# Optimization experiments

Measured on AMD Instinct MI355X. Metric: run time of the kernel, lower is better.

## Reference

```python
import jax, jax.numpy as jnp
import numpy as np


def gcn_conv(x, W, b, src, dst, n):
    # GCNConv with self-loops and symmetric normalization:
    # out_i = sum_{j in N(i)} (deg_i*deg_j)^{-1/2} (x_j W) + deg_i^{-1} (x_i W) + b
    h = x @ W                                   # [n, H]
    deg = jnp.zeros((n,), h.dtype).at[dst].add(1.0) + 1.0  # +1 self-loop
    dinv = jax.lax.rsqrt(deg)                   # deg^{-1/2}
    norm = dinv[src] * dinv[dst]                # [E]
    msg = h[src] * norm[:, None]                # [E, H] gathered/scaled messages
    agg = jax.ops.segment_sum(msg, dst, num_segments=n)
    agg = agg + h * (dinv * dinv)[:, None]      # self-loop contribution
    return agg + b


def global_mean_pool(x, batch, num_graphs):
    s = jax.ops.segment_sum(x, batch, num_segments=num_graphs)
    cnt = jax.ops.segment_sum(jnp.ones((x.shape[0],), x.dtype), batch, num_segments=num_graphs)
    return s / jnp.maximum(cnt, 1.0)[:, None]


def setup_inputs() -> dict:
    key = jax.random.key(0)
    ks = jax.random.split(key, 8)
    N, E, F, H, G = 100000, 1600000, 128, 128, 512
    x = jax.random.normal(ks[0], (N, F), dtype=jnp.float32)
    edge_index = jax.random.randint(ks[1], (2, E), 0, N, dtype=jnp.int64)
    batch = jnp.sort(jax.random.randint(ks[2], (N,), 0, G, dtype=jnp.int64))
    W1 = jax.random.normal(ks[3], (F, H), dtype=jnp.float32) / np.sqrt(F)
    b1 = jnp.zeros((H,), jnp.float32)
    W2 = jax.random.normal(ks[4], (H, H), dtype=jnp.float32) / np.sqrt(H)
    b2 = jnp.zeros((H,), jnp.float32)
    Wlin = jax.random.normal(ks[5], (H, 1), dtype=jnp.float32) / np.sqrt(H)
    blin = jnp.zeros((1,), jnp.float32)
    return {"x": x, "W1": W1, "b1": b1, "W2": W2, "b2": b2,
            "Wlin": Wlin, "blin": blin,
            "edge_index": edge_index, "batch": batch, "num_graphs": G}


def reference(x, W1, b1, W2, b2, Wlin, blin, edge_index, batch, num_graphs):
    n = x.shape[0]
    src, dst = edge_index[0], edge_index[1]
    h = jax.nn.relu(gcn_conv(x, W1, b1, src, dst, n))
    h = jax.nn.relu(gcn_conv(h, W2, b2, src, dst, n))
    g = global_mean_pool(h, batch, num_graphs)   # [G, H]
    return g @ Wlin + blin                       # [G, 1]
```

## Files before the change

kernel.cpp:

```cpp
#include <hip/hip_runtime.h>
#include <hip/hip_bf16.h>


#define NBS 7
#define NPB 128
#define PART_TILE 4096
#define BCAP 3072

typedef __attribute__((ext_vector_type(8))) short short8;
typedef __attribute__((ext_vector_type(4))) float f32x4;

__device__ __forceinline__ float bf2f(unsigned short u) {
    return __uint_as_float(((unsigned int)u) << 16);
}
__device__ __forceinline__ unsigned short f2bf(float f) {
    unsigned int u = __float_as_uint(f);
    return (unsigned short)((u + 0x7FFFu + ((u >> 16) & 1u)) >> 16);
}
__device__ __forceinline__ short8 pack_bf8(f32x4 a, f32x4 b) {
    short8 s;
    s[0] = (short)f2bf(a.x); s[1] = (short)f2bf(a.y);
    s[2] = (short)f2bf(a.z); s[3] = (short)f2bf(a.w);
    s[4] = (short)f2bf(b.x); s[5] = (short)f2bf(b.y);
    s[6] = (short)f2bf(b.z); s[7] = (short)f2bf(b.w);
    return s;
}
__device__ __forceinline__ void acc8(int4 v, float* a) {
    a[0] += __uint_as_float(((unsigned int)v.x) << 16);
    a[1] += __uint_as_float(((unsigned int)v.x) & 0xFFFF0000u);
    a[2] += __uint_as_float(((unsigned int)v.y) << 16);
    a[3] += __uint_as_float(((unsigned int)v.y) & 0xFFFF0000u);
    a[4] += __uint_as_float(((unsigned int)v.z) << 16);
    a[5] += __uint_as_float(((unsigned int)v.z) & 0xFFFF0000u);
    a[6] += __uint_as_float(((unsigned int)v.w) << 16);
    a[7] += __uint_as_float(((unsigned int)v.w) & 0xFFFF0000u);
}
__device__ __forceinline__ unsigned int pack2(float x, float y) {
    return (unsigned int)f2bf(x) | ((unsigned int)f2bf(y) << 16);
}


__global__ __launch_bounds__(256) void partition_kernel(const int* __restrict__ src,
                                                        const int* __restrict__ dst, int E,
                                                        int* __restrict__ bcur,
                                                        unsigned int* __restrict__ pairs,
                                                        int B) {
    __shared__ int h[1024];
    __shared__ int rankbase[1024];
    int t = threadIdx.x;
    int tile0 = blockIdx.x * PART_TILE;
    for (int i = t; i < B; i += 256) h[i] = 0;
    __syncthreads();

    int bk[16];
    int rk[16];
    unsigned int pk[16];
#pragma unroll
    for (int j = 0; j < 16; ++j) {
        int idx = tile0 + j * 256 + t;
        bk[j] = -1;
        if (idx < E) {
            int d = dst[idx];
            int s = src[idx];
            bk[j] = d >> NBS;
            pk[j] = ((unsigned int)(d & (NPB - 1)) << 23) | (unsigned int)s;
            rk[j] = atomicAdd(&h[bk[j]], 1);
        }
    }
    __syncthreads();
    for (int i = t; i < B; i += 256) rankbase[i] = h[i] ? atomicAdd(&bcur[i], h[i]) : 0;
    __syncthreads();
#pragma unroll
    for (int j = 0; j < 16; ++j)
        if (bk[j] >= 0) pairs[rankbase[bk[j]] + rk[j]] = pk[j];
}

__global__ __launch_bounds__(256) void bucket_finalize(const unsigned int* __restrict__ pairs,
                                                       const int* __restrict__ bcur,
                                                       int* __restrict__ rps,
                                                       int* __restrict__ rpe,
                                                       float* __restrict__ dinv,
                                                       int* __restrict__ col, int N) {
    __shared__ int c[NPB];
    __shared__ int sa[NPB];
    __shared__ int sb[NPB];
    __shared__ unsigned int stage[BCAP];
    int b = blockIdx.x;
    int s = b * BCAP;
    int cnt = bcur[b] - s;
    if (threadIdx.x < NPB) c[threadIdx.x] = 0;
    __syncthreads();
    for (int i = threadIdx.x; i < cnt; i += 256) {
        unsigned int p = pairs[s + i];
        stage[i] = p;
        atomicAdd(&c[p >> 23], 1);
    }
    __syncthreads();
    if (threadIdx.x < NPB) sa[threadIdx.x] = c[threadIdx.x];
    __syncthreads();
    int* pin = sa;
    int* pout = sb;
    for (int off = 1; off < NPB; off <<= 1) {
        if (threadIdx.x < NPB)
            pout[threadIdx.x] = pin[threadIdx.x] + ((threadIdx.x >= (unsigned)off) ? pin[threadIdx.x - off] : 0);
        __syncthreads();
        int* tmp = pin; pin = pout; pout = tmp;
    }
    int base = b << NBS;
    if (threadIdx.x < NPB) {
        int i = threadIdx.x;
        int excl = s + pin[i] - c[i];
        pout[i] = excl;
        int node = base + i;
        if (node < N) {
            rps[node] = excl;
            rpe[node] = excl + c[i];
            dinv[node] = rsqrtf((float)c[i] + 1.0f);
        }
    }
    __syncthreads();
    for (int i = threadIdx.x; i < cnt; i += 256) {
        unsigned int p = stage[i];
        int dL = (int)(p >> 23);
        int pos = atomicAdd(&pout[dL], 1);
        col[pos] = (int)(p & 0x7FFFFFu);
    }
}


__global__ void wconv_kernel(const float* __restrict__ W1, const float* __restrict__ W2,
                             unsigned short* __restrict__ Wt1, unsigned short* __restrict__ Wt2,
                             int* __restrict__ bcur, int B,
                             float* __restrict__ ps, int psn) {
    const float* W = (blockIdx.x & 128) ? W2 : W1;
    unsigned short* Wt = (blockIdx.x & 128) ? Wt2 : Wt1;
    int n = blockIdx.x & 127;
    int k = threadIdx.x;
    Wt[n * 128 + k] = f2bf(W[k * 128 + n]);
    int tid = blockIdx.x * 128 + threadIdx.x;
    if (tid < B) bcur[tid] = tid * BCAP;
    for (int i = tid; i < psn; i += 256 * 128) ps[i] = 0.f;
}


template <bool A_F32>
__global__ __launch_bounds__(256) void gemm_mfma(const void* __restrict__ Ap,
                                                 const unsigned short* __restrict__ Wt,
                                                 const float* __restrict__ dinv,
                                                 unsigned short* __restrict__ C, int M) {
    __shared__ unsigned char lds[32768];
    int t = threadIdx.x;
#pragma unroll
    for (int i = 0; i < 8; ++i) {
        int c = t + i * 256;
        int row = c >> 4;
        int b = (c & 15) << 4;
        int4 v = ((const int4*)Wt)[c];
        *(int4*)&lds[row * 256 + (b ^ ((row & 7) << 4))] = v;
    }

    int lane = t & 63;
    int wv = t >> 6;
    int r0 = blockIdx.x * 64 + wv * 16;
    int l15 = lane & 15;
    int kg = lane >> 4;

    short8 af[4];
    {
        int row = r0 + l15;
        row = row < M ? row : M - 1;
#pragma unroll
        for (int kk = 0; kk < 4; ++kk) {
            size_t eoff = (size_t)row * 128 + kk * 32 + kg * 8;
            if constexpr (A_F32) {
                const float* A = (const float*)Ap;
                f32x4 v0 = __builtin_nontemporal_load((const f32x4*)(A + eoff));
                f32x4 v1 = __builtin_nontemporal_load((const f32x4*)(A + eoff + 4));
                af[kk] = pack_bf8(v0, v1);
            } else {
                af[kk] = *(const short8*)((const unsigned short*)Ap + eoff);
            }
        }
    }
    __syncthreads();

    f32x4 acc[8];
#pragma unroll
    for (int cf = 0; cf < 8; ++cf) acc[cf] = (f32x4)(0.f);

#pragma unroll
    for (int cf = 0; cf < 8; ++cf) {
        short8 bfr[4];
#pragma unroll
        for (int kk = 0; kk < 4; ++kk) {
            int brow = cf * 16 + l15;
            int bb = kk * 64 + kg * 16;
            bfr[kk] = *(const short8*)&lds[brow * 256 + (bb ^ ((brow & 7) << 4))];
        }
#pragma unroll
        for (int kk = 0; kk < 4; ++kk)
            acc[cf] = __builtin_amdgcn_mfma_f32_16x16x32_bf16(af[kk], bfr[kk], acc[cf], 0, 0, 0);
    }

#pragma unroll
    for (int r = 0; r < 4; ++r) {
        int row = r0 + kg * 4 + r;
        if (row < M) {
            float dv = dinv[row];
#pragma unroll
            for (int cf = 0; cf < 8; ++cf)
                C[(size_t)row * 128 + cf * 16 + l15] = f2bf(acc[cf][r] * dv);
        }
    }
}


template <bool FUSE_POOL>
__global__ __launch_bounds__(256) void agg_q16(const unsigned short* __restrict__ hs,
                                               const float* __restrict__ dinv,
                                               const int* __restrict__ rps,
                                               const int* __restrict__ rpe,
                                               const int* __restrict__ col,
                                               const float* __restrict__ bias,
                                               const int* __restrict__ batch,
                                               unsigned short* __restrict__ out,
                                               float* __restrict__ ps, int N) {
    int slot = threadIdx.x >> 4;
    int g = blockIdx.x * 16 + slot;
    int l = threadIdx.x & 15;
    bool valid = (g < N);
    if (!FUSE_POOL && !valid) return;

    float a[8];
#pragma unroll
    for (int k = 0; k < 8; ++k) a[k] = 0.f;

    if (valid) {
        const int4* h4 = (const int4*)hs;
        {
            int4 sv = h4[(size_t)g * 16 + l];
            acc8(sv, a);
        }
        int e = rps[g], end = rpe[g];
        for (; e + 7 < end; e += 8) {
            int j0 = col[e + 0], j1 = col[e + 1], j2 = col[e + 2], j3 = col[e + 3];
            int j4 = col[e + 4], j5 = col[e + 5], j6 = col[e + 6], j7 = col[e + 7];
            int4 v0 = h4[(size_t)j0 * 16 + l];
            int4 v1 = h4[(size_t)j1 * 16 + l];
            int4 v2 = h4[(size_t)j2 * 16 + l];
            int4 v3 = h4[(size_t)j3 * 16 + l];
            int4 v4 = h4[(size_t)j4 * 16 + l];
            int4 v5 = h4[(size_t)j5 * 16 + l];
            int4 v6 = h4[(size_t)j6 * 16 + l];
            int4 v7 = h4[(size_t)j7 * 16 + l];
            acc8(v0, a); acc8(v1, a); acc8(v2, a); acc8(v3, a);
            acc8(v4, a); acc8(v5, a); acc8(v6, a); acc8(v7, a);
        }
        for (; e + 1 < end; e += 2) {
            int j0 = col[e], j1 = col[e + 1];
            int4 v0 = h4[(size_t)j0 * 16 + l];
            int4 v1 = h4[(size_t)j1 * 16 + l];
            acc8(v0, a); acc8(v1, a);
        }
        if (e < end) {
            int j = col[e];
            acc8(h4[(size_t)j * 16 + l], a);
        }

        float dv = dinv[g];
        float4 b0 = ((const float4*)bias)[l * 2];
        float4 b1 = ((const float4*)bias)[l * 2 + 1];
        a[0] = fmaxf(fmaf(a[0], dv, b0.x), 0.f);
        a[1] = fmaxf(fmaf(a[1], dv, b0.y), 0.f);
        a[2] = fmaxf(fmaf(a[2], dv, b0.z), 0.f);
        a[3] = fmaxf(fmaf(a[3], dv, b0.w), 0.f);
        a[4] = fmaxf(fmaf(a[4], dv, b1.x), 0.f);
        a[5] = fmaxf(fmaf(a[5], dv, b1.y), 0.f);
        a[6] = fmaxf(fmaf(a[6], dv, b1.z), 0.f);
        a[7] = fmaxf(fmaf(a[7], dv, b1.w), 0.f);
    }

    if constexpr (FUSE_POOL) {
        __shared__ float sacc[16][128];
        __shared__ int sbatch[16];
        if (l == 0) sbatch[slot] = valid ? batch[g] : -1;
#pragma unroll
        for (int k = 0; k < 8; ++k) sacc[slot][l * 8 + k] = a[k];
        __syncthreads();
        if (threadIdx.x < 128) {
            int f = threadIdx.x;
            float run = 0.f;
            int curg = sbatch[0];
#pragma unroll
            for (int s2 = 0; s2 < 16; ++s2) {
                int gg = sbatch[s2];
                if (gg < 0) break;
                if (gg != curg) {
                    atomicAdd(&ps[curg * 128 + f], run);
                    run = 0.f;
                    curg = gg;
                }
                run += sacc[s2][f];
            }
            if (curg >= 0) atomicAdd(&ps[curg * 128 + f], run);
        }
    } else {
        int4 o;
        o.x = (int)pack2(a[0], a[1]);
        o.y = (int)pack2(a[2], a[3]);
        o.z = (int)pack2(a[4], a[5]);
        o.w = (int)pack2(a[6], a[7]);
        ((int4*)out)[(size_t)g * 16 + l] = o;
    }
}

__global__ __launch_bounds__(256) void final_kernel(const float* __restrict__ ps,
                                                    const int* __restrict__ batch, int N,
                                                    const float* __restrict__ Wlin,
                                                    const float* __restrict__ blin,
                                                    float* __restrict__ out, int G) {
    int g = (int)((blockIdx.x * 256 + threadIdx.x) >> 6);
    int lane = threadIdx.x & 63;
    if (g >= G) return;
    float2 s = ((const float2*)ps)[g * 64 + lane];
    float2 w = ((const float2*)Wlin)[lane];
    float v = s.x * w.x + s.y * w.y;
#pragma unroll
    for (int off = 32; off > 0; off >>= 1) v += __shfl_down(v, off);
    if (lane == 0) {
        int lo = 0, hi = N;
        while (lo < hi) { int m = (lo + hi) >> 1; if (batch[m] < g) lo = m + 1; else hi = m; }
        int lb = lo;
        hi = N;
        while (lo < hi) { int m = (lo + hi) >> 1; if (batch[m] <= g) lo = m + 1; else hi = m; }
        float c = (float)max(lo - lb, 1);
        out[g] = v / c + blin[0];
    }
}

extern "C" void kernel_launch(void* const* d_in, const int* in_sizes, int n_in,
                              void* d_out, int out_size, void* d_ws, size_t ws_size,
                              hipStream_t stream) {
    const float* x    = (const float*)d_in[0];
    const float* W1   = (const float*)d_in[1];
    const float* b1   = (const float*)d_in[2];
    const float* W2   = (const float*)d_in[3];
    const float* b2   = (const float*)d_in[4];
    const float* Wlin = (const float*)d_in[5];
    const float* blin = (const float*)d_in[6];
    const int*   ei   = (const int*)d_in[7];
    const int*   batch= (const int*)d_in[8];

    const int N = in_sizes[0] / 128;
    const int E = in_sizes[7] / 2;
    const int G = out_size;
    const int B = (N + NPB - 1) >> NBS;

    const int* srcp = ei;
    const int* dstp = ei + E;

    char* w = (char*)d_ws;
    size_t off = 0;
    auto carve = [&](size_t bytes) {
        size_t o = off;
        off = (off + bytes + 255) & ~(size_t)255;
        return (void*)(w + o);
    };
    unsigned short* bufA = (unsigned short*)carve((size_t)N * 128 * 2);
    unsigned short* bufB = (unsigned short*)carve((size_t)N * 128 * 2);
    float* dinv = (float*)carve((size_t)N * 4);
    int*   rps  = (int*)carve((size_t)N * 4);
    int*   rpe  = (int*)carve((size_t)N * 4);
    int*   col  = (int*)carve((size_t)B * BCAP * 4);
    unsigned int* pairs = (unsigned int*)carve((size_t)B * BCAP * 4);
    int*   bcur = (int*)carve((size_t)(B + 1) * 4);
    unsigned short* Wt1 = (unsigned short*)carve(128 * 128 * 2);
    unsigned short* Wt2 = (unsigned short*)carve(128 * 128 * 2);
    float* ps   = (float*)carve((size_t)G * 128 * 4);
    (void)ws_size;

    const int ntiles = (E + PART_TILE - 1) / PART_TILE;

    wconv_kernel<<<256, 128, 0, stream>>>(W1, W2, Wt1, Wt2, bcur, B, ps, G * 128);

    partition_kernel<<<ntiles, 256, 0, stream>>>(srcp, dstp, E, bcur, pairs, B);
    bucket_finalize<<<B, 256, 0, stream>>>(pairs, bcur, rps, rpe, dinv, col, N);

    const int gemm_grid = (N + 63) / 64;
    const int agg_grid  = (N + 15) / 16;

    gemm_mfma<true><<<gemm_grid, 256, 0, stream>>>(x, Wt1, dinv, bufA, N);
    agg_q16<false><<<agg_grid, 256, 0, stream>>>(bufA, dinv, rps, rpe, col, b1, batch, bufB, ps, N);
    gemm_mfma<false><<<gemm_grid, 256, 0, stream>>>(bufB, Wt2, dinv, bufA, N);
    agg_q16<true><<<agg_grid, 256, 0, stream>>>(bufA, dinv, rps, rpe, col, b2, batch, bufB, ps, N);

    final_kernel<<<(G * 64 + 255) / 256, 256, 0, stream>>>(ps, batch, N, Wlin, blin,
                                                           (float*)d_out, G);
}
```

Baseline: 214.1 us.

## Fuse layer-1 aggregation with layer-2 GEMM and double partition tile

Layer-1 neighbour aggregation and the layer-2 MFMA GEMM now run in one kernel. Each block aggregates 16 nodes into LDS as bf16 and multiplies them by W2, with the B fragments read straight from global memory. This removes a separate GEMM launch and a full N×128 bf16 write and re-read of the intermediate activations. The partition kernel also processes two 4096-edge halves per block, halving the number of blocks and their per-block setup. The cost is that every fused block reloads all of W2 from global memory, and the partition blocks serialise their two halves.

```diff
diff --git a/kernel.cpp b/kernel.cpp
--- a/kernel.cpp
+++ b/kernel.cpp
@@ -4,7 +4,7 @@
 
 #define NBS 7
 #define NPB 128
-#define PART_TILE 4096
+#define PART_TILE 8192
 #define BCAP 3072
 
 typedef __attribute__((ext_vector_type(8))) short short8;
@@ -39,6 +39,51 @@
     return (unsigned int)f2bf(x) | ((unsigned int)f2bf(y) << 16);
 }
 
+__device__ __forceinline__ void gather_relu(const unsigned short* __restrict__ hs,
+                                            const float* __restrict__ dinv,
+                                            const int* __restrict__ rps,
+                                            const int* __restrict__ rpe,
+                                            const int* __restrict__ col,
+                                            const float* __restrict__ bias,
+                                            int g, int l, float* a) {
+    const int4* h4 = (const int4*)hs;
+    acc8(h4[(size_t)g * 16 + l], a);
+    int e = rps[g], end = rpe[g];
+    for (; e + 7 < end; e += 8) {
+        int j0 = col[e + 0], j1 = col[e + 1], j2 = col[e + 2], j3 = col[e + 3];
+        int j4 = col[e + 4], j5 = col[e + 5], j6 = col[e + 6], j7 = col[e + 7];
+        int4 v0 = h4[(size_t)j0 * 16 + l];
+        int4 v1 = h4[(size_t)j1 * 16 + l];
+        int4 v2 = h4[(size_t)j2 * 16 + l];
+        int4 v3 = h4[(size_t)j3 * 16 + l];
+        int4 v4 = h4[(size_t)j4 * 16 + l];
+        int4 v5 = h4[(size_t)j5 * 16 + l];
+        int4 v6 = h4[(size_t)j6 * 16 + l];
+        int4 v7 = h4[(size_t)j7 * 16 + l];
+        acc8(v0, a); acc8(v1, a); acc8(v2, a); acc8(v3, a);
+        acc8(v4, a); acc8(v5, a); acc8(v6, a); acc8(v7, a);
+    }
+    for (; e + 1 < end; e += 2) {
+        int j0 = col[e], j1 = col[e + 1];
+        int4 v0 = h4[(size_t)j0 * 16 + l];
+        int4 v1 = h4[(size_t)j1 * 16 + l];
+        acc8(v0, a); acc8(v1, a);
+    }
+    if (e < end) acc8(h4[(size_t)col[e] * 16 + l], a);
+
+    float dv = dinv[g];
+    float4 b0 = ((const float4*)bias)[l * 2];
+    float4 b1 = ((const float4*)bias)[l * 2 + 1];
+    a[0] = fmaxf(fmaf(a[0], dv, b0.x), 0.f);
+    a[1] = fmaxf(fmaf(a[1], dv, b0.y), 0.f);
+    a[2] = fmaxf(fmaf(a[2], dv, b0.z), 0.f);
+    a[3] = fmaxf(fmaf(a[3], dv, b0.w), 0.f);
+    a[4] = fmaxf(fmaf(a[4], dv, b1.x), 0.f);
+    a[5] = fmaxf(fmaf(a[5], dv, b1.y), 0.f);
+    a[6] = fmaxf(fmaf(a[6], dv, b1.z), 0.f);
+    a[7] = fmaxf(fmaf(a[7], dv, b1.w), 0.f);
+}
+
 
 __global__ __launch_bounds__(256) void partition_kernel(const int* __restrict__ src,
                                                         const int* __restrict__ dst, int E,
@@ -49,30 +94,34 @@
     __shared__ int rankbase[1024];
     int t = threadIdx.x;
     int tile0 = blockIdx.x * PART_TILE;
-    for (int i = t; i < B; i += 256) h[i] = 0;
-    __syncthreads();
-
-    int bk[16];
-    int rk[16];
-    unsigned int pk[16];
-#pragma unroll
-    for (int j = 0; j < 16; ++j) {
-        int idx = tile0 + j * 256 + t;
-        bk[j] = -1;
-        if (idx < E) {
-            int d = dst[idx];
-            int s = src[idx];
-            bk[j] = d >> NBS;
-            pk[j] = ((unsigned int)(d & (NPB - 1)) << 23) | (unsigned int)s;
-            rk[j] = atomicAdd(&h[bk[j]], 1);
-        }
-    }
-    __syncthreads();
-    for (int i = t; i < B; i += 256) rankbase[i] = h[i] ? atomicAdd(&bcur[i], h[i]) : 0;
-    __syncthreads();
-#pragma unroll
-    for (int j = 0; j < 16; ++j)
-        if (bk[j] >= 0) pairs[rankbase[bk[j]] + rk[j]] = pk[j];
+
+    for (int half = 0; half < 2; ++half) {
+        for (int i = t; i < B; i += 256) h[i] = 0;
+        __syncthreads();
+        int base0 = tile0 + half * 4096;
+        int bk[16];
+        int rk[16];
+        unsigned int pk[16];
+#pragma unroll
+        for (int j = 0; j < 16; ++j) {
+            int idx = base0 + j * 256 + t;
+            bk[j] = -1;
+            if (idx < E) {
+                int d = dst[idx];
+                int s = src[idx];
+                bk[j] = d >> NBS;
+                pk[j] = ((unsigned int)(d & (NPB - 1)) << 23) | (unsigned int)s;
+                rk[j] = atomicAdd(&h[bk[j]], 1);
+            }
+        }
+        __syncthreads();
+        for (int i = t; i < B; i += 256) rankbase[i] = h[i] ? atomicAdd(&bcur[i], h[i]) : 0;
+        __syncthreads();
+#pragma unroll
+        for (int j = 0; j < 16; ++j)
+            if (bk[j] >= 0) pairs[rankbase[bk[j]] + rk[j]] = pk[j];
+        __syncthreads();
+    }
 }
 
 __global__ __launch_bounds__(256) void bucket_finalize(const unsigned int* __restrict__ pairs,
@@ -143,8 +192,7 @@
 }
 
 
-template <bool A_F32>
-__global__ __launch_bounds__(256) void gemm_mfma(const void* __restrict__ Ap,
+__global__ __launch_bounds__(256) void gemm_mfma(const float* __restrict__ A,
                                                  const unsigned short* __restrict__ Wt,
                                                  const float* __restrict__ dinv,
                                                  unsigned short* __restrict__ C, int M) {
@@ -172,14 +220,9 @@
 #pragma unroll
         for (int kk = 0; kk < 4; ++kk) {
             size_t eoff = (size_t)row * 128 + kk * 32 + kg * 8;
-            if constexpr (A_F32) {
-                const float* A = (const float*)Ap;
-                f32x4 v0 = __builtin_nontemporal_load((const f32x4*)(A + eoff));
-                f32x4 v1 = __builtin_nontemporal_load((const f32x4*)(A + eoff + 4));
-                af[kk] = pack_bf8(v0, v1);
-            } else {
-                af[kk] = *(const short8*)((const unsigned short*)Ap + eoff);
-            }
+            f32x4 v0 = __builtin_nontemporal_load((const f32x4*)(A + eoff));
+            f32x4 v1 = __builtin_nontemporal_load((const f32x4*)(A + eoff + 4));
+            af[kk] = pack_bf8(v0, v1);
         }
     }
     __syncthreads();
@@ -215,102 +258,104 @@
 }
 
 
-template <bool FUSE_POOL>
-__global__ __launch_bounds__(256) void agg_q16(const unsigned short* __restrict__ hs,
-                                               const float* __restrict__ dinv,
-                                               const int* __restrict__ rps,
-                                               const int* __restrict__ rpe,
-                                               const int* __restrict__ col,
-                                               const float* __restrict__ bias,
-                                               const int* __restrict__ batch,
-                                               unsigned short* __restrict__ out,
-                                               float* __restrict__ ps, int N) {
+__global__ __launch_bounds__(256) void agg1_gemm2(const unsigned short* __restrict__ hs,
+                                                  const float* __restrict__ dinv,
+                                                  const int* __restrict__ rps,
+                                                  const int* __restrict__ rpe,
+                                                  const int* __restrict__ col,
+                                                  const float* __restrict__ b1,
+                                                  const unsigned short* __restrict__ Wt2,
+                                                  unsigned short* __restrict__ hs2, int N) {
+    __shared__ unsigned char sacc[16 * 256];
     int slot = threadIdx.x >> 4;
     int g = blockIdx.x * 16 + slot;
     int l = threadIdx.x & 15;
     bool valid = (g < N);
-    if (!FUSE_POOL && !valid) return;
 
     float a[8];
 #pragma unroll
     for (int k = 0; k < 8; ++k) a[k] = 0.f;
-
-    if (valid) {
-        const int4* h4 = (const int4*)hs;
-        {
-            int4 sv = h4[(size_t)g * 16 + l];
-            acc8(sv, a);
-        }
-        int e = rps[g], end = rpe[g];
-        for (; e + 7 < end; e += 8) {
-            int j0 = col[e + 0], j1 = col[e + 1], j2 = col[e + 2], j3 = col[e + 3];
-            int j4 = col[e + 4], j5 = col[e + 5], j6 = col[e + 6], j7 = col[e + 7];
-            int4 v0 = h4[(size_t)j0 * 16 + l];
-            int4 v1 = h4[(size_t)j1 * 16 + l];
-            int4 v2 = h4[(size_t)j2 * 16 + l];
-            int4 v3 = h4[(size_t)j3 * 16 + l];
-            int4 v4 = h4[(size_t)j4 * 16 + l];
-            int4 v5 = h4[(size_t)j5 * 16 + l];
-            int4 v6 = h4[(size_t)j6 * 16 + l];
-            int4 v7 = h4[(size_t)j7 * 16 + l];
-            acc8(v0, a); acc8(v1, a); acc8(v2, a); acc8(v3, a);
-            acc8(v4, a); acc8(v5, a); acc8(v6, a); acc8(v7, a);
-        }
-        for (; e + 1 < end; e += 2) {
-            int j0 = col[e], j1 = col[e + 1];
-            int4 v0 = h4[(size_t)j0 * 16 + l];
-            int4 v1 = h4[(size_t)j1 * 16 + l];
-            acc8(v0, a); acc8(v1, a);
-        }
-        if (e < end) {
-            int j = col[e];
-            acc8(h4[(size_t)j * 16 + l], a);
-        }
-
-        float dv = dinv[g];
-        float4 b0 = ((const float4*)bias)[l * 2];
-        float4 b1 = ((const float4*)bias)[l * 2 + 1];
-        a[0] = fmaxf(fmaf(a[0], dv, b0.x), 0.f);
-        a[1] = fmaxf(fmaf(a[1], dv, b0.y), 0.f);
-        a[2] = fmaxf(fmaf(a[2], dv, b0.z), 0.f);
-        a[3] = fmaxf(fmaf(a[3], dv, b0.w), 0.f);
-        a[4] = fmaxf(fmaf(a[4], dv, b1.x), 0.f);
-        a[5] = fmaxf(fmaf(a[5], dv, b1.y), 0.f);
-        a[6] = fmaxf(fmaf(a[6], dv, b1.z), 0.f);
-        a[7] = fmaxf(fmaf(a[7], dv, b1.w), 0.f);
-    }
-
-    if constexpr (FUSE_POOL) {
-        __shared__ float sacc[16][128];
-        __shared__ int sbatch[16];
-        if (l == 0) sbatch[slot] = valid ? batch[g] : -1;
-#pragma unroll
-        for (int k = 0; k < 8; ++k) sacc[slot][l * 8 + k] = a[k];
-        __syncthreads();
-        if (threadIdx.x < 128) {
-            int f = threadIdx.x;
-            float run = 0.f;
-            int curg = sbatch[0];
-#pragma unroll
-            for (int s2 = 0; s2 < 16; ++s2) {
-                int gg = sbatch[s2];
-                if (gg < 0) break;
-                if (gg != curg) {
-                    atomicAdd(&ps[curg * 128 + f], run);
-                    run = 0.f;
-                    curg = gg;
-                }
-                run += sacc[s2][f];
+    if (valid) gather_relu(hs, dinv, rps, rpe, col, b1, g, l, a);
+
+    int4 o;
+    o.x = (int)pack2(a[0], a[1]);
+    o.y = (int)pack2(a[2], a[3]);
+    o.z = (int)pack2(a[4], a[5]);
+    o.w = (int)pack2(a[6], a[7]);
+    *(int4*)&sacc[slot * 256 + ((l * 16) ^ ((slot & 7) << 4))] = o;
+    __syncthreads();
+
+    int lane = threadIdx.x & 63;
+    int wv = threadIdx.x >> 6;
+    int l15 = lane & 15;
+    int kg = lane >> 4;
+
+    short8 af[4];
+#pragma unroll
+    for (int kk = 0; kk < 4; ++kk) {
+        int bb = kk * 64 + kg * 16;
+        af[kk] = *(const short8*)&sacc[l15 * 256 + (bb ^ ((l15 & 7) << 4))];
+    }
+
+#pragma unroll
+    for (int c2 = 0; c2 < 2; ++c2) {
+        int cf = wv * 2 + c2;
+        f32x4 acc = (f32x4)(0.f);
+#pragma unroll
+        for (int kk = 0; kk < 4; ++kk) {
+            short8 bfr = *(const short8*)&Wt2[(size_t)(cf * 16 + l15) * 128 + kk * 32 + kg * 8];
+            acc = __builtin_amdgcn_mfma_f32_16x16x32_bf16(af[kk], bfr, acc, 0, 0, 0);
+        }
+#pragma unroll
+        for (int r = 0; r < 4; ++r) {
+            int row = blockIdx.x * 16 + kg * 4 + r;
+            if (row < N)
+                hs2[(size_t)row * 128 + cf * 16 + l15] = f2bf(acc[r] * dinv[row]);
+        }
+    }
+}
+
+
+__global__ __launch_bounds__(256) void agg_pool(const unsigned short* __restrict__ hs,
+                                                const float* __restrict__ dinv,
+                                                const int* __restrict__ rps,
+                                                const int* __restrict__ rpe,
+                                                const int* __restrict__ col,
+                                                const float* __restrict__ bias,
+                                                const int* __restrict__ batch,
+                                                float* __restrict__ ps, int N) {
+    __shared__ float sacc[16][128];
+    __shared__ int sbatch[16];
+    int slot = threadIdx.x >> 4;
+    int g = blockIdx.x * 16 + slot;
+    int l = threadIdx.x & 15;
+    bool valid = (g < N);
+
+    float a[8];
+#pragma unroll
+    for (int k = 0; k < 8; ++k) a[k] = 0.f;
+    if (valid) gather_relu(hs, dinv, rps, rpe, col, bias, g, l, a);
+
+    if (l == 0) sbatch[slot] = valid ? batch[g] : -1;
+#pragma unroll
+    for (int k = 0; k < 8; ++k) sacc[slot][l * 8 + k] = a[k];
+    __syncthreads();
+    if (threadIdx.x < 128) {
+        int f = threadIdx.x;
+        float run = 0.f;
+        int curg = sbatch[0];
+#pragma unroll
+        for (int s2 = 0; s2 < 16; ++s2) {
+            int gg = sbatch[s2];
+            if (gg < 0) break;
+            if (gg != curg) {
+                atomicAdd(&ps[curg * 128 + f], run);
+                run = 0.f;
+                curg = gg;
             }
-            if (curg >= 0) atomicAdd(&ps[curg * 128 + f], run);
-        }
-    } else {
-        int4 o;
-        o.x = (int)pack2(a[0], a[1]);
-        o.y = (int)pack2(a[2], a[3]);
-        o.z = (int)pack2(a[4], a[5]);
-        o.w = (int)pack2(a[6], a[7]);
-        ((int4*)out)[(size_t)g * 16 + l] = o;
+            run += sacc[s2][f];
+        }
+        if (curg >= 0) atomicAdd(&ps[curg * 128 + f], run);
     }
 }
 
@@ -389,10 +434,9 @@
     const int gemm_grid = (N + 63) / 64;
     const int agg_grid  = (N + 15) / 16;
 
-    gemm_mfma<true><<<gemm_grid, 256, 0, stream>>>(x, Wt1, dinv, bufA, N);
-    agg_q16<false><<<agg_grid, 256, 0, stream>>>(bufA, dinv, rps, rpe, col, b1, batch, bufB, ps, N);
-    gemm_mfma<false><<<gemm_grid, 256, 0, stream>>>(bufB, Wt2, dinv, bufA, N);
-    agg_q16<true><<<agg_grid, 256, 0, stream>>>(bufA, dinv, rps, rpe, col, b2, batch, bufB, ps, N);
+    gemm_mfma<<<gemm_grid, 256, 0, stream>>>(x, Wt1, dinv, bufA, N);
+    agg1_gemm2<<<agg_grid, 256, 0, stream>>>(bufA, dinv, rps, rpe, col, b1, Wt2, bufB, N);
+    agg_pool<<<agg_grid, 256, 0, stream>>>(bufB, dinv, rps, rpe, col, b2, batch, ps, N);
 
     final_kernel<<<(G * 64 + 255) / 256, 256, 0, stream>>>(ps, batch, N, Wlin, blin,
                                                            (float*)d_out, G);
```

New measurement: 223.0 us. 4.2% more time.
